# Performance work log

Hardware: AMD Instinct MI355X
Metric: run time of the kernel (lower is better)

Reference implementation:

```python
import jax, jax.numpy as jnp
import numpy as np

N_SITE, N_VENDOR, E = 100000, 20000, 3200000
SITE_IN, VENDOR_IN, HID, OUT = 10, 9, 64, 32


def _sage(x_src, x_dst, src, dst, n_dst, Wl, bl, Wr):
    # PyG SAGEConv (mean aggr): lin_l(mean_{e: dst(e)=i} x_src[src(e)]) + lin_r(x_dst)
    msg = x_src[src]                                   # [E, d] gather
    agg = jax.ops.segment_sum(msg, dst, num_segments=n_dst)
    cnt = jax.ops.segment_sum(jnp.ones((src.shape[0],), x_src.dtype), dst,
                              num_segments=n_dst)
    mean = agg / jnp.maximum(cnt, 1.0)[:, None]
    return mean @ Wl + bl + x_dst @ Wr


def setup_inputs() -> dict:
    key = jax.random.key(0)
    ks = jax.random.split(key, 24)
    g = lambda k, s: (jax.random.normal(k, s, jnp.float32) / np.sqrt(s[0])).astype(jnp.float32)
    inp = {
        'x_site': jax.random.normal(ks[0], (N_SITE, SITE_IN), jnp.float32),
        'x_vendor': jax.random.normal(ks[1], (N_VENDOR, VENDOR_IN), jnp.float32),
        'src': jax.random.randint(ks[2], (E,), 0, N_SITE),
        'dst': jax.random.randint(ks[3], (E,), 0, N_VENDOR),
        # input projections
        'W_site_in': g(ks[4], (SITE_IN, HID)), 'b_site_in': jnp.zeros((HID,), jnp.float32),
        'W_vendor_in': g(ks[5], (VENDOR_IN, HID)), 'b_vendor_in': jnp.zeros((HID,), jnp.float32),
        # conv1 site->vendor (64->64)
        'Wl1sv': g(ks[6], (HID, HID)), 'bl1sv': jnp.zeros((HID,), jnp.float32), 'Wr1sv': g(ks[7], (HID, HID)),
        # conv1 vendor->site (64->64)
        'Wl1vs': g(ks[8], (HID, HID)), 'bl1vs': jnp.zeros((HID,), jnp.float32), 'Wr1vs': g(ks[9], (HID, HID)),
        # conv2 site->vendor (64->32)
        'Wl2sv': g(ks[10], (HID, OUT)), 'bl2sv': jnp.zeros((OUT,), jnp.float32), 'Wr2sv': g(ks[11], (HID, OUT)),
        # conv2 vendor->site (64->32)
        'Wl2vs': g(ks[12], (HID, OUT)), 'bl2vs': jnp.zeros((OUT,), jnp.float32), 'Wr2vs': g(ks[13], (HID, OUT)),
    }
    return inp


def reference(x_site, x_vendor, src, dst,
              W_site_in, b_site_in, W_vendor_in, b_vendor_in,
              Wl1sv, bl1sv, Wr1sv, Wl1vs, bl1vs, Wr1vs,
              Wl2sv, bl2sv, Wr2sv, Wl2vs, bl2vs, Wr2vs):
    xs = x_site @ W_site_in + b_site_in        # [N_SITE, HID]
    xv = x_vendor @ W_vendor_in + b_vendor_in  # [N_VENDOR, HID]
    # layer 1 (dropout is identity in eval mode)
    xv1 = jax.nn.relu(_sage(xs, xv, src, dst, N_VENDOR, Wl1sv, bl1sv, Wr1sv))
    xs1 = jax.nn.relu(_sage(xv, xs, dst, src, N_SITE, Wl1vs, bl1vs, Wr1vs))
    # layer 2
    xv2 = jax.nn.relu(_sage(xs1, xv1, src, dst, N_VENDOR, Wl2sv, bl2sv, Wr2sv))
    xs2 = jax.nn.relu(_sage(xv1, xs1, dst, src, N_SITE, Wl2vs, bl2vs, Wr2vs))
    # concat [site; vendor] -> [N_SITE + N_VENDOR, OUT]
    return jnp.concatenate([xs2, xv2], axis=0)
```

## Files before the change

### kernel.cpp

```cpp
#include <hip/hip_runtime.h>

constexpr int N_SITE    = 100000;
constexpr int N_VENDOR  = 20000;
constexpr int NE        = 3200000;
constexpr int SITE_IN   = 10;
constexpr int VENDOR_IN = 9;
constexpr int HID       = 64;
constexpr int OUT       = 32;

constexpr int NBLK    = 256;
constexpr int EPB     = NE / NBLK;
constexpr int SHIFT_S = 7;
constexpr int NBUK_S  = (N_SITE + 127) / 128;
constexpr int CAP_S   = 5120;
constexpr int SHIFT_V = 6;
constexpr int NBUK_V  = (N_VENDOR + 63) / 64;
constexpr int CAP_V   = 12288;

constexpr int SB1  = (N_SITE + 3) / 4;
constexpr int VB1  = (N_VENDOR + 3) / 4;
constexpr int NS_BLK = (N_SITE + 15) / 16;
constexpr int NV_BLK = (N_VENDOR + 15) / 16;
constexpr int PADTOT = 16 * (N_SITE + N_VENDOR);

constexpr long long I_NSTART_S = 0;
constexpr long long I_NDEG_S   = I_NSTART_S + N_SITE;
constexpr long long I_NSTART_V = I_NDEG_S + N_SITE;
constexpr long long I_NDEG_V   = I_NSTART_V + N_VENDOR;
constexpr long long I_GCUR     = I_NDEG_V + N_VENDOR;
constexpr long long I_ADJ_V    = (I_GCUR + NBUK_S + NBUK_V + 3) & ~3LL;
constexpr long long I_ADJ_S    = I_ADJ_V + (long long)NBUK_V * CAP_V;
constexpr long long INT_END    = (I_ADJ_S + (long long)NBUK_S * CAP_S / 2 + 3) & ~3LL;
constexpr long long A_PAIRS_S  = INT_END;
constexpr long long A_PAIRS_V  = A_PAIRS_S + (long long)NBUK_S * CAP_S;
constexpr long long BUILD_END  = A_PAIRS_V + (long long)NBUK_V * CAP_V;
constexpr long long F_Y16    = (BUILD_END + 3) & ~3LL;
constexpr long long F_PAD    = F_Y16 + (long long)(N_SITE + N_VENDOR) * 16;
constexpr long long F_FUSED  = F_PAD + (long long)(N_SITE + N_VENDOR) * 8;
constexpr long long WS_WORDS = F_FUSED + 4352;

constexpr int F_M1SV = 0;
constexpr int F_M1VS = 1024;
constexpr int F_R1SV = 2048;
constexpr int F_R1VS = 3072;
constexpr int F_V1SV = 4096;
constexpr int F_V1VS = 4160;
constexpr int F_r1SV = 4224;
constexpr int F_r1VS = 4288;

typedef _Float16 h2_t __attribute__((ext_vector_type(2)));
__device__ __forceinline__ h2_t as_h2(unsigned u) {
    union { unsigned u; h2_t h; } c; c.u = u; return c.h;
}
__device__ __forceinline__ unsigned short f2h(float f) {
    union { _Float16 h; unsigned short u; } c; c.h = (_Float16)f; return c.u;
}
#if defined(__has_builtin)
#if __has_builtin(__builtin_amdgcn_fdot2)
#define HAVE_FDOT2 1
#endif
#endif
__device__ __forceinline__ void acc2(float& slo, float& shi, unsigned u) {
#ifdef HAVE_FDOT2
    h2_t sel_lo = {(_Float16)1.0f, (_Float16)0.0f};
    h2_t sel_hi = {(_Float16)0.0f, (_Float16)1.0f};
    slo = __builtin_amdgcn_fdot2(as_h2(u), sel_lo, slo, false);
    shi = __builtin_amdgcn_fdot2(as_h2(u), sel_hi, shi, false);
#else
    h2_t h = as_h2(u);
    slo += (float)h.x; shi += (float)h.y;
#endif
}
__device__ __forceinline__ float ddot2(unsigned a, unsigned b, float c) {
#ifdef HAVE_FDOT2
    return __builtin_amdgcn_fdot2(as_h2(a), as_h2(b), c, false);
#else
    h2_t ha = as_h2(a), hb = as_h2(b);
    return c + (float)ha.x * (float)hb.x + (float)ha.y * (float)hb.y;
#endif
}

__global__ __launch_bounds__(256) void prep(
        const float* __restrict__ x_site, const float* __restrict__ x_vendor,
        unsigned short* __restrict__ xsp, unsigned short* __restrict__ xvp,
        const float* __restrict__ Wsi, const float* __restrict__ bsi,
        const float* __restrict__ Wvi, const float* __restrict__ bvi,
        const float* __restrict__ Wl1sv, const float* __restrict__ Wr1sv,
        const float* __restrict__ Wl1vs, const float* __restrict__ Wr1vs,
        float* __restrict__ fused) {
    long long t = (long long)blockIdx.x * 256 + threadIdx.x;
    if (t < (long long)N_SITE * 16) {
        int i = (int)(t >> 4), k = (int)(t & 15);
        xsp[t] = f2h(k < SITE_IN ? x_site[i * SITE_IN + k] : 0.f);
        return;
    }
    t -= (long long)N_SITE * 16;
    if (t < (long long)N_VENDOR * 16) {
        int i = (int)(t >> 4), k = (int)(t & 15);
        xvp[t] = f2h(k < VENDOR_IN ? x_vendor[i * VENDOR_IN + k] : 0.f);
        return;
    }
    t -= (long long)N_VENDOR * 16;
    int idx = (int)t;
    if (idx < 4096) {
        int m = idx >> 10, rem = idx & 1023, r = rem >> 6, c = rem & 63;
        int K = (m == 0 || m == 3) ? SITE_IN : VENDOR_IN;
        const float* A = (m == 0 || m == 3) ? Wsi : Wvi;
        const float* B = (m == 0) ? Wl1sv : (m == 1) ? Wl1vs : (m == 2) ? Wr1sv : Wr1vs;
        float s = 0.f;
        if (r < K)
            for (int j = 0; j < 64; ++j) s = fmaf(A[r * 64 + j], B[j * 64 + c], s);
        fused[idx] = s;
    } else if (idx < 4352) {
        int m = (idx - 4096) >> 6, c = idx & 63;
        const float* a = (m == 0 || m == 3) ? bsi : bvi;
        const float* B = (m == 0) ? Wl1sv : (m == 1) ? Wl1vs : (m == 2) ? Wr1sv : Wr1vs;
        float s = 0.f;
        for (int j = 0; j < 64; ++j) s = fmaf(a[j], B[j * 64 + c], s);
        fused[idx] = s;
    }
}

__global__ __launch_bounds__(256) void scatter_res(
        const int* __restrict__ src, const int* __restrict__ dst,
        int* __restrict__ gcur,
        unsigned* __restrict__ pairs_s, unsigned* __restrict__ pairs_v) {
    __shared__ int hs[NBUK_S];
    __shared__ int hv[NBUK_V];
    int blk = blockIdx.x, tid = threadIdx.x;
    for (int i = tid; i < NBUK_S; i += 256) hs[i] = 0;
    for (int i = tid; i < NBUK_V; i += 256) hv[i] = 0;
    __syncthreads();
    int lo = blk * EPB;
    for (int e = lo + tid; e < lo + EPB; e += 256) {
        atomicAdd(&hs[src[e] >> SHIFT_S], 1);
        atomicAdd(&hv[dst[e] >> SHIFT_V], 1);
    }
    __syncthreads();
    for (int i = tid; i < NBUK_S; i += 256) {
        int c = hs[i];
        hs[i] = c ? atomicAdd(&gcur[i], c) : 0;
    }
    for (int i = tid; i < NBUK_V; i += 256) {
        int c = hv[i];
        hv[i] = c ? atomicAdd(&gcur[NBUK_S + i], c) : 0;
    }
    __syncthreads();
    for (int e = lo + tid; e < lo + EPB; e += 256) {
        int s = src[e], d = dst[e];
        int bs = s >> SHIFT_S;
        int ps = atomicAdd(&hs[bs], 1);
        if (ps < CAP_S)
            pairs_s[(long long)bs * CAP_S + ps] =
                ((unsigned)(s & 127) << 25) | (unsigned)d;
        int bv = d >> SHIFT_V;
        int pv = atomicAdd(&hv[bv], 1);
        if (pv < CAP_V)
            pairs_v[(long long)bv * CAP_V + pv] =
                ((unsigned)(d & 63) << 26) | (unsigned)s;
    }
}

__global__ __launch_bounds__(256) void stage2both(
        const unsigned* __restrict__ pairs_s, const unsigned* __restrict__ pairs_v,
        const int* __restrict__ gcur,
        int* __restrict__ nstart_s, int* __restrict__ ndeg_s,
        int* __restrict__ nstart_v, int* __restrict__ ndeg_v,
        unsigned short* __restrict__ adj_s16, int* __restrict__ adj_v) {
    int b = blockIdx.x, tid = threadIdx.x;
    bool site = (b < NBUK_S);
    const unsigned* pairs; int *nst, *ndg;
    int BW, nnode, shloc, lo_node, cnt;
    long long p0;
    if (site) {
        pairs = pairs_s; nst = nstart_s; ndg = ndeg_s;
        BW = 128; nnode = N_SITE; shloc = 25; lo_node = b << SHIFT_S;
        p0 = (long long)b * CAP_S;
        cnt = min(gcur[b], CAP_S);
    } else {
        b -= NBUK_S;
        pairs = pairs_v; nst = nstart_v; ndg = ndeg_v;
        BW = 64; nnode = N_VENDOR; shloc = 26; lo_node = b << SHIFT_V;
        p0 = (long long)b * CAP_V;
        cnt = min(gcur[NBUK_S + b], CAP_V);
    }
    long long p1 = p0 + cnt;
    __shared__ int deg[128];
    __shared__ int cur[128];
    __shared__ int sc[256];
    if (tid < BW) deg[tid] = 0;
    __syncthreads();
    for (long long e = p0 + tid; e < p1; e += 256)
        atomicAdd(&deg[(int)(pairs[e] >> shloc)], 1);
    __syncthreads();
    int d = (tid < BW) ? deg[tid] : 0;
    sc[tid] = d;
    __syncthreads();
    for (int st = 1; st < 256; st <<= 1) {
        int x = (tid >= st) ? sc[tid - st] : 0; __syncthreads();
        sc[tid] += x; __syncthreads();
    }
    int excl = sc[tid] - d;
    if (tid < BW) {
        int node = lo_node + tid;
        if (node < nnode) {
            nst[node] = (int)(p0 + excl);
            ndg[node] = d;
        }
        cur[tid] = (int)(p0 + excl);
    }
    __syncthreads();
    if (site) {
        for (long long e = p0 + tid; e < p1; e += 256) {
            unsigned p = pairs[e];
            int pos = atomicAdd(&cur[(int)(p >> 25)], 1);
            adj_s16[pos] = (unsigned short)p;
        }
    } else {
        for (long long e = p0 + tid; e < p1; e += 256) {
            unsigned p = pairs[e];
            int pos = atomicAdd(&cur[(int)(p >> 26)], 1);
            adj_v[pos] = (int)(p & 0x3FFFFFFu);
        }
    }
}

template<typename IdxT>
__device__ __forceinline__ void gather1x(const unsigned short* __restrict__ fp,
                                         const IdxT* __restrict__ adj,
                                         int lo, int hi, int l16, float* s) {
    for (int j = lo + l16; j < hi; j += 16) {
        const unsigned short* row = fp + (long long)adj[j] * 16;
        uint4 q0 = *(const uint4*)row;
        unsigned u4 = *(const unsigned*)(row + 8);
        acc2(s[0], s[1], q0.x);
        acc2(s[2], s[3], q0.y);
        acc2(s[4], s[5], q0.z);
        acc2(s[6], s[7], q0.w);
        acc2(s[8], s[9], u4);
    }
}

__global__ __launch_bounds__(256) void gc1fused(
        const unsigned short* __restrict__ xsp, const unsigned short* __restrict__ xvp,
        const float* __restrict__ xs_raw, const float* __restrict__ xv_raw,
        const int* __restrict__ nstart_s, const int* __restrict__ ndeg_s,
        const unsigned short* __restrict__ adj_s16,
        const int* __restrict__ nstart_v, const int* __restrict__ ndeg_v,
        const int* __restrict__ adj_v,
        const float* __restrict__ fused,
        const float* __restrict__ bl1vs, const float* __restrict__ bl1sv,
        const float* __restrict__ Wl2sv, const float* __restrict__ Wr2vs,
        const float* __restrict__ Wl2vs, const float* __restrict__ Wr2sv,
        unsigned short* __restrict__ ys16, unsigned short* __restrict__ yv16,
        float* __restrict__ out) {
    __shared__ unsigned sWp[32 * 64];
    __shared__ unsigned sXp[16][34];
    int b = blockIdx.x, tid = threadIdx.x;
    bool site = (b < NS_BLK);
    const float *fsraw, *M, *V, *BL, *R, *RV, *Wl, *Wr;
    const int *nst, *ndg;
    unsigned short* Y; float* Z;
    int nodebase, n, kx;
    if (site) {
        nodebase = b * 16; n = N_SITE; kx = SITE_IN;
        fsraw = xs_raw; nst = nstart_s; ndg = ndeg_s;
        M = fused + F_M1VS; V = fused + F_V1VS; BL = bl1vs;
        R = fused + F_R1VS; RV = fused + F_r1VS;
        Wl = Wl2sv; Wr = Wr2vs; Y = ys16; Z = out;
    } else {
        nodebase = (b - NS_BLK) * 16; n = N_VENDOR; kx = VENDOR_IN;
        fsraw = xv_raw; nst = nstart_v; ndg = ndeg_v;
        M = fused + F_M1SV; V = fused + F_V1SV; BL = bl1sv;
        R = fused + F_R1SV; RV = fused + F_r1SV;
        Wl = Wl2vs; Wr = Wr2sv; Y = yv16;
        Z = out + (long long)N_SITE * OUT;
    }
    for (int i = tid; i < 2048; i += 256) {
        int kk = i >> 6, c = i & 63;
        int k0 = kk * 2, k1 = k0 + 1;
        float w0 = (c < 32) ? Wl[k0 * 32 + c] : Wr[k0 * 32 + (c - 32)];
        float w1 = (c < 32) ? Wl[k1 * 32 + c] : Wr[k1 * 32 + (c - 32)];
        sWp[i] = (unsigned)f2h(w0) | ((unsigned)f2h(w1) << 16);
    }
    int l16 = tid & 15, nib = tid >> 4;
    int w = nodebase + nib;
    int c0 = l16 * 4;
    if (w < n) {
        int lo = nst[w], deg = ndg[w], hi = lo + deg;
        float s[10];
        #pragma unroll
        for (int k = 0; k < 10; ++k) s[k] = 0.f;
        if (site) gather1x(xvp, adj_s16, lo, hi, l16, s);
        else      gather1x(xsp, adj_v,   lo, hi, l16, s);
        #pragma unroll
        for (int k = 0; k < 10; ++k) {
            s[k] += __shfl_xor(s[k], 1, 64);
            s[k] += __shfl_xor(s[k], 2, 64);
            s[k] += __shfl_xor(s[k], 4, 64);
            s[k] += __shfl_xor(s[k], 8, 64);
        }
        float inv = 1.0f / (float)max(deg, 1);
        float4 acc = *(const float4*)(BL + c0);
        float4 rv4 = *(const float4*)(RV + c0);
        acc.x += rv4.x; acc.y += rv4.y; acc.z += rv4.z; acc.w += rv4.w;
        if (deg > 0) {
            float4 v4 = *(const float4*)(V + c0);
            acc.x += v4.x; acc.y += v4.y; acc.z += v4.z; acc.w += v4.w;
        }
        #pragma unroll
        for (int k = 0; k < 10; ++k) {
            float m = s[k] * inv;
            float4 m4 = *(const float4*)(M + k * 64 + c0);
            acc.x = fmaf(m, m4.x, acc.x);
            acc.y = fmaf(m, m4.y, acc.y);
            acc.z = fmaf(m, m4.z, acc.z);
            acc.w = fmaf(m, m4.w, acc.w);
        }
        const float* xr = fsraw + (long long)w * kx;
        for (int k = 0; k < kx; ++k) {
            float xv = xr[k];
            float4 r4 = *(const float4*)(R + k * 64 + c0);
            acc.x = fmaf(xv, r4.x, acc.x);
            acc.y = fmaf(xv, r4.y, acc.y);
            acc.z = fmaf(xv, r4.z, acc.z);
            acc.w = fmaf(xv, r4.w, acc.w);
        }
        unsigned plo = (unsigned)f2h(fmaxf(acc.x, 0.f)) |
                       ((unsigned)f2h(fmaxf(acc.y, 0.f)) << 16);
        unsigned phi = (unsigned)f2h(fmaxf(acc.z, 0.f)) |
                       ((unsigned)f2h(fmaxf(acc.w, 0.f)) << 16);
        *(uint2*)&sXp[nib][l16 * 2] = make_uint2(plo, phi);
    }
    __syncthreads();
    int n2 = tid >> 4, q = tid & 15;
    int node = nodebase + n2;
    float4 acc = {0.f, 0.f, 0.f, 0.f};
    const unsigned* xrow = sXp[n2];
    #pragma unroll 8
    for (int kk = 0; kk < 32; ++kk) {
        unsigned xp = xrow[kk];
        uint4 wp = *(const uint4*)(sWp + kk * 64 + q * 4);
        acc.x = ddot2(xp, wp.x, acc.x);
        acc.y = ddot2(xp, wp.y, acc.y);
        acc.z = ddot2(xp, wp.z, acc.z);
        acc.w = ddot2(xp, wp.w, acc.w);
    }
    if (node < n) {
        if (q < 8) {
            unsigned p01 = (unsigned)f2h(acc.x) | ((unsigned)f2h(acc.y) << 16);
            unsigned p23 = (unsigned)f2h(acc.z) | ((unsigned)f2h(acc.w) << 16);
            *(uint2*)(Y + (long long)node * 32 + q * 4) = make_uint2(p01, p23);
        } else {
            *(float4*)(Z + (long long)node * 32 + (q - 8) * 4) = acc;
        }
    }
}

template<typename IdxT>
__device__ __forceinline__ void gather2(const unsigned short* __restrict__ y,
                                        const IdxT* __restrict__ adj,
                                        int lo, int deg, int g, int q,
                                        float& s0, float& s1, float& s2, float& s3) {
    int m = (deg > g) ? ((deg - g + 7) >> 3) : 0;
    const IdxT* ap = adj + lo + g;
    int t = 0;
    for (; t + 4 <= m; t += 4) {
        long long a0 = (long long)ap[8 * t];
        long long a1 = (long long)ap[8 * t + 8];
        long long a2 = (long long)ap[8 * t + 16];
        long long a3 = (long long)ap[8 * t + 24];
        uint2 u0 = *(const uint2*)(y + a0 * 32 + 4 * q);
        uint2 u1 = *(const uint2*)(y + a1 * 32 + 4 * q);
        uint2 u2 = *(const uint2*)(y + a2 * 32 + 4 * q);
        uint2 u3 = *(const uint2*)(y + a3 * 32 + 4 * q);
        acc2(s0, s1, u0.x); acc2(s2, s3, u0.y);
        acc2(s0, s1, u1.x); acc2(s2, s3, u1.y);
        acc2(s0, s1, u2.x); acc2(s2, s3, u2.y);
        acc2(s0, s1, u3.x); acc2(s2, s3, u3.y);
    }
    for (; t < m; ++t) {
        long long a0 = (long long)ap[8 * t];
        uint2 u0 = *(const uint2*)(y + a0 * 32 + 4 * q);
        acc2(s0, s1, u0.x); acc2(s2, s3, u0.y);
    }
}

__global__ __launch_bounds__(256) void gc2all(
        const unsigned short* __restrict__ ys16, const unsigned short* __restrict__ yv16,
        const int* __restrict__ nstart_s, const int* __restrict__ ndeg_s,
        const unsigned short* __restrict__ adj_s16,
        const int* __restrict__ nstart_v, const int* __restrict__ ndeg_v,
        const int* __restrict__ adj_v,
        const float* __restrict__ bl2vs, const float* __restrict__ bl2sv,
        float* __restrict__ out) {
    int b = blockIdx.x;
    bool site = (b < SB1);
    const float* bias; const int *nst, *ndg; float* o; int w, n;
    if (site) {
        w = b * 4 + (threadIdx.x >> 6); n = N_SITE;
        nst = nstart_s; ndg = ndeg_s; bias = bl2vs; o = out;
    } else {
        w = (b - SB1) * 4 + (threadIdx.x >> 6); n = N_VENDOR;
        nst = nstart_v; ndg = ndeg_v; bias = bl2sv;
        o = out + (long long)N_SITE * OUT;
    }
    if (w >= n) return;
    int lane = threadIdx.x & 63, g = lane >> 3, q = lane & 7;
    int lo = nst[w], deg = ndg[w];
    float s0 = 0.f, s1 = 0.f, s2 = 0.f, s3 = 0.f;
    if (site) gather2(yv16, adj_s16, lo, deg, g, q, s0, s1, s2, s3);
    else      gather2(ys16, adj_v,   lo, deg, g, q, s0, s1, s2, s3);
    #pragma unroll
    for (int m = 8; m <= 32; m <<= 1) {
        s0 += __shfl_xor(s0, m, 64);
        s1 += __shfl_xor(s1, m, 64);
        s2 += __shfl_xor(s2, m, 64);
        s3 += __shfl_xor(s3, m, 64);
    }
    if (g == 0) {
        float inv = 1.0f / (float)max(deg, 1);
        float4 bz = *(const float4*)(bias + 4 * q);
        long long oi = (long long)w * 32 + 4 * q;
        float4 z = *(const float4*)(o + oi);
        float4 r;
        r.x = fmaxf(fmaf(s0, inv, bz.x + z.x), 0.f);
        r.y = fmaxf(fmaf(s1, inv, bz.y + z.y), 0.f);
        r.z = fmaxf(fmaf(s2, inv, bz.z + z.z), 0.f);
        r.w = fmaxf(fmaf(s3, inv, bz.w + z.w), 0.f);
        *(float4*)(o + oi) = r;
    }
}

extern "C" void kernel_launch(void* const* d_in, const int* in_sizes, int n_in,
                              void* d_out, int out_size, void* d_ws, size_t ws_size,
                              hipStream_t stream) {
    const float* x_site      = (const float*)d_in[0];
    const float* x_vendor    = (const float*)d_in[1];
    const int*   src         = (const int*)d_in[2];
    const int*   dst         = (const int*)d_in[3];
    const float* W_site_in   = (const float*)d_in[4];
    const float* b_site_in   = (const float*)d_in[5];
    const float* W_vendor_in = (const float*)d_in[6];
    const float* b_vendor_in = (const float*)d_in[7];
    const float* Wl1sv = (const float*)d_in[8];
    const float* bl1sv = (const float*)d_in[9];
    const float* Wr1sv = (const float*)d_in[10];
    const float* Wl1vs = (const float*)d_in[11];
    const float* bl1vs = (const float*)d_in[12];
    const float* Wr1vs = (const float*)d_in[13];
    const float* Wl2sv = (const float*)d_in[14];
    const float* bl2sv = (const float*)d_in[15];
    const float* Wr2sv = (const float*)d_in[16];
    const float* Wl2vs = (const float*)d_in[17];
    const float* bl2vs = (const float*)d_in[18];
    const float* Wr2vs = (const float*)d_in[19];

    if (ws_size < (size_t)WS_WORDS * 4) return;

    int*   wi  = (int*)d_ws;
    float* wf  = (float*)d_ws;
    float* out = (float*)d_out;

    int* nstart_s = wi + I_NSTART_S;
    int* ndeg_s   = wi + I_NDEG_S;
    int* nstart_v = wi + I_NSTART_V;
    int* ndeg_v   = wi + I_NDEG_V;
    int* gcur     = wi + I_GCUR;
    int* adj_v    = wi + I_ADJ_V;
    unsigned short* adj_s16 = (unsigned short*)(wi + I_ADJ_S);
    unsigned* pairs_s = (unsigned*)(wi + A_PAIRS_S);
    unsigned* pairs_v = (unsigned*)(wi + A_PAIRS_V);
    unsigned short* ys16 = (unsigned short*)(wf + F_Y16);
    unsigned short* yv16 = ys16 + (long long)N_SITE * 32;
    unsigned short* xsp  = (unsigned short*)(wf + F_PAD);
    unsigned short* xvp  = xsp + (long long)N_SITE * 16;
    float* fused = wf + F_FUSED;

    hipMemsetAsync(gcur, 0, (size_t)(NBUK_S + NBUK_V) * sizeof(int), stream);

    prep<<<(PADTOT + 4352 + 255) / 256, 256, 0, stream>>>(
        x_site, x_vendor, xsp, xvp,
        W_site_in, b_site_in, W_vendor_in, b_vendor_in,
        Wl1sv, Wr1sv, Wl1vs, Wr1vs, fused);

    scatter_res<<<NBLK, 256, 0, stream>>>(src, dst, gcur, pairs_s, pairs_v);
    stage2both<<<NBUK_S + NBUK_V, 256, 0, stream>>>(pairs_s, pairs_v, gcur,
                                                    nstart_s, ndeg_s,
                                                    nstart_v, ndeg_v,
                                                    adj_s16, adj_v);

    gc1fused<<<NS_BLK + NV_BLK, 256, 0, stream>>>(
        xsp, xvp, x_site, x_vendor,
        nstart_s, ndeg_s, adj_s16, nstart_v, ndeg_v, adj_v,
        fused, bl1vs, bl1sv, Wl2sv, Wr2vs, Wl2vs, Wr2sv,
        ys16, yv16, out);

    gc2all<<<SB1 + VB1, 256, 0, stream>>>(ys16, yv16,
                                          nstart_s, ndeg_s, adj_s16,
                                          nstart_v, ndeg_v, adj_v,
                                          bl2vs, bl2sv, out);

    (void)in_sizes; (void)n_in; (void)out_size;
}
```

Measured before the change: 292.0 us.

## Sort edge pairs by bucket in LDS before writing to global buckets

Replaces the direct per-edge scatter of packed pairs with a block-local counting sort in shared memory. Each direction's keys are histogrammed, prefix-scanned into local offsets and staged in an LDS buffer, then written out so consecutive threads store contiguous runs within each bucket. The aim is to turn scattered global stores into mostly coalesced ones. The cost is a larger LDS footprint, a serial pass per direction that re-reads src and dst, extra barriers and a binary search per element to find its bucket.

```diff
diff --git a/kernel.cpp b/kernel.cpp
--- a/kernel.cpp
+++ b/kernel.cpp
@@ -121,43 +121,78 @@
     }
 }
 
-__global__ __launch_bounds__(256) void scatter_res(
+__global__ __launch_bounds__(256) void scatter_sort(
         const int* __restrict__ src, const int* __restrict__ dst,
         int* __restrict__ gcur,
         unsigned* __restrict__ pairs_s, unsigned* __restrict__ pairs_v) {
-    __shared__ int hs[NBUK_S];
-    __shared__ int hv[NBUK_V];
+    __shared__ unsigned buf[EPB];
+    __shared__ int hcnt[NBUK_S];
+    __shared__ int loff[NBUK_S + 1];
+    __shared__ int gbase[NBUK_S];
+    __shared__ int sc[256];
     int blk = blockIdx.x, tid = threadIdx.x;
-    for (int i = tid; i < NBUK_S; i += 256) hs[i] = 0;
-    for (int i = tid; i < NBUK_V; i += 256) hv[i] = 0;
-    __syncthreads();
     int lo = blk * EPB;
-    for (int e = lo + tid; e < lo + EPB; e += 256) {
-        atomicAdd(&hs[src[e] >> SHIFT_S], 1);
-        atomicAdd(&hv[dst[e] >> SHIFT_V], 1);
-    }
-    __syncthreads();
-    for (int i = tid; i < NBUK_S; i += 256) {
-        int c = hs[i];
-        hs[i] = c ? atomicAdd(&gcur[i], c) : 0;
-    }
-    for (int i = tid; i < NBUK_V; i += 256) {
-        int c = hv[i];
-        hv[i] = c ? atomicAdd(&gcur[NBUK_S + i], c) : 0;
-    }
-    __syncthreads();
-    for (int e = lo + tid; e < lo + EPB; e += 256) {
-        int s = src[e], d = dst[e];
-        int bs = s >> SHIFT_S;
-        int ps = atomicAdd(&hs[bs], 1);
-        if (ps < CAP_S)
-            pairs_s[(long long)bs * CAP_S + ps] =
-                ((unsigned)(s & 127) << 25) | (unsigned)d;
-        int bv = d >> SHIFT_V;
-        int pv = atomicAdd(&hv[bv], 1);
-        if (pv < CAP_V)
-            pairs_v[(long long)bv * CAP_V + pv] =
-                ((unsigned)(d & 63) << 26) | (unsigned)s;
+    #pragma unroll 1
+    for (int dir = 0; dir < 2; ++dir) {
+        const int nbuk  = dir ? NBUK_V : NBUK_S;
+        const int shift = dir ? SHIFT_V : SHIFT_S;
+        const int* key  = dir ? dst : src;
+        const int* val  = dir ? src : dst;
+        const int goff  = dir ? NBUK_S : 0;
+        const long long cap = dir ? CAP_V : CAP_S;
+        unsigned* pairs = dir ? pairs_v : pairs_s;
+        for (int i = tid; i < nbuk; i += 256) hcnt[i] = 0;
+        __syncthreads();
+        for (int e = lo + tid; e < lo + EPB; e += 256)
+            atomicAdd(&hcnt[key[e] >> shift], 1);
+        __syncthreads();
+        int base_i = tid * 4;
+        int c4[4], s = 0;
+        #pragma unroll
+        for (int k = 0; k < 4; ++k) {
+            int i = base_i + k;
+            int c = (i < nbuk) ? hcnt[i] : 0;
+            c4[k] = s; s += c;
+        }
+        sc[tid] = s; __syncthreads();
+        for (int st = 1; st < 256; st <<= 1) {
+            int x = (tid >= st) ? sc[tid - st] : 0; __syncthreads();
+            sc[tid] += x; __syncthreads();
+        }
+        int pre = tid ? sc[tid - 1] : 0;
+        #pragma unroll
+        for (int k = 0; k < 4; ++k) {
+            int i = base_i + k;
+            if (i < nbuk) loff[i] = pre + c4[k];
+        }
+        if (tid == 0) loff[nbuk] = EPB;
+        __syncthreads();
+        for (int i = tid; i < nbuk; i += 256) {
+            int c = hcnt[i];
+            gbase[i] = c ? atomicAdd(&gcur[goff + i], c) : 0;
+        }
+        __syncthreads();
+        for (int i = tid; i < nbuk; i += 256) hcnt[i] = loff[i];
+        __syncthreads();
+        for (int e = lo + tid; e < lo + EPB; e += 256) {
+            int kk = key[e], vv = val[e];
+            int b = kk >> shift;
+            int p = atomicAdd(&hcnt[b], 1);
+            buf[p] = dir ? (((unsigned)(kk & 63) << 26) | (unsigned)vv)
+                         : (((unsigned)(kk & 127) << 25) | (unsigned)vv);
+        }
+        __syncthreads();
+        for (int t = tid; t < EPB; t += 256) {
+            int lb = 0, hb = nbuk;
+            while (hb - lb > 1) {
+                int mid = (lb + hb) >> 1;
+                if (loff[mid] <= t) lb = mid; else hb = mid;
+            }
+            int rel = gbase[lb] + (t - loff[lb]);
+            if (rel < (int)cap)
+                pairs[(long long)lb * cap + rel] = buf[t];
+        }
+        __syncthreads();
     }
 }
 
@@ -484,7 +519,7 @@
         W_site_in, b_site_in, W_vendor_in, b_vendor_in,
         Wl1sv, Wr1sv, Wl1vs, Wr1vs, fused);
 
-    scatter_res<<<NBLK, 256, 0, stream>>>(src, dst, gcur, pairs_s, pairs_v);
+    scatter_sort<<<NBLK, 256, 0, stream>>>(src, dst, gcur, pairs_s, pairs_v);
     stage2both<<<NBUK_S + NBUK_V, 256, 0, stream>>>(pairs_s, pairs_v, gcur,
                                                     nstart_s, ndeg_s,
                                                     nstart_v, ndeg_v,
```

Result: slower. 346.0 us (+18.5%).
